# Performance work log

Hardware: AMD Instinct MI355X
Metric: run time of the kernel (lower is better)

The kernel has to match this reference:

```python
import jax, jax.numpy as jnp
import numpy as np

N_NODES = 16384
D_FEAT = 128
HIDDEN = 64
THRESH = 0.85


def setup_inputs() -> dict:
    key = jax.random.key(0)
    kx, kw = jax.random.split(key, 2)
    x = jax.random.normal(kx, (N_NODES, D_FEAT), dtype=jnp.float32)
    # nn.Linear(node_features, hidden_size): weight [H, D], bias [H]
    W = jax.random.normal(kw, (HIDDEN, D_FEAT), dtype=jnp.float32) * 0.05
    b = jnp.zeros((HIDDEN,), dtype=jnp.float32)
    return {"x": x, "W": W, "b": b}


def reference(x, W, b):
    n = x.shape[0]
    # fidelity = (x_i . x_j)^2 for all pairs  -> [n, n]
    fid = jnp.square(x @ x.T)
    # edges exist iff fid >= threshold (weight 1.0); the 0.5-weight elif branch
    # in the original is unreachable. No self-loops (j starts at i+1).
    adj = (fid >= THRESH).astype(x.dtype)
    idx = jnp.arange(n)
    adj = adj.at[idx, idx].set(0.0)
    # weighted neighbor sum per node: [n, d]
    sums = adj @ x
    # original assigns agg[node] = (weights @ neighbor_feats).mean(), a SCALAR
    # broadcast across the feature row; isolated nodes stay zero (their sum
    # row is already zero, so mean is zero -> identical result).
    agg = jnp.broadcast_to(jnp.mean(sums, axis=-1, keepdims=True), x.shape)
    return agg @ W.T + b
```

## Files before the change

kernel.cpp:

```cpp
#include <hip/hip_runtime.h>

#define N_NODES 16384
#define D_FEAT  128
#define HIDDEN  64
#define THRESH  0.85f
#define BAND    0.004f
#define LQCAP   512
#define NBLK    512
#define NT      64

typedef __attribute__((ext_vector_type(8))) short bf16x8;
typedef __attribute__((ext_vector_type(4))) float f32x4;

__device__ __forceinline__ unsigned short f32_to_bf16_rne(float f) {
    unsigned u = __float_as_uint(f);
    unsigned r = (u + 0x7FFFu + ((u >> 16) & 1u)) >> 16;
    return (unsigned short)r;
}

__device__ __forceinline__ void gl_lds16(const unsigned short* src, unsigned short* dst) {
    __builtin_amdgcn_global_load_lds(
        (const __attribute__((address_space(1))) unsigned int*)src,
        (__attribute__((address_space(3))) unsigned int*)dst, 16, 0, 0);
}

__global__ __launch_bounds__(256) void convert_rowsum_kernel(const float* __restrict__ x,
                                                             unsigned short* __restrict__ xhi,
                                                             unsigned short* __restrict__ xlo,
                                                             float* __restrict__ s,
                                                             float* __restrict__ acc,
                                                             int* __restrict__ qcnt) {
    const int tid  = threadIdx.x;
    const int gidx = blockIdx.x * 256 + tid;
    float4 v = ((const float4*)x)[gidx];
    float f[4] = {v.x, v.y, v.z, v.w};
    ushort4 ho, lo;
    unsigned short* hp = &ho.x;
    unsigned short* lp = &lo.x;
    #pragma unroll
    for (int k = 0; k < 4; ++k) {
        unsigned short h = f32_to_bf16_rne(f[k]);
        float hf = __uint_as_float(((unsigned)h) << 16);
        hp[k] = h;
        lp[k] = f32_to_bf16_rne(f[k] - hf);
    }
    ((ushort4*)xhi)[gidx] = ho;
    ((ushort4*)xlo)[gidx] = lo;

    float sum = (v.x + v.y) + (v.z + v.w);
    #pragma unroll
    for (int off = 16; off > 0; off >>= 1) sum += __shfl_xor(sum, off);
    if ((tid & 31) == 0) s[blockIdx.x * 8 + (tid >> 5)] = sum;

    if (tid < 8) acc[blockIdx.x * 8 + tid] = 0.0f;
    if (gidx == 0) *qcnt = 0;
}

__global__ __launch_bounds__(256) void rowsum_kernel(const float* __restrict__ in,
                                                     float* __restrict__ out,
                                                     int nrows) {
    int wave = (blockIdx.x * blockDim.x + threadIdx.x) >> 6;
    int lane = threadIdx.x & 63;
    if (wave >= nrows) return;
    const float2 v = *reinterpret_cast<const float2*>(&in[wave * D_FEAT + lane * 2]);
    float sum = v.x + v.y;
    #pragma unroll
    for (int off = 32; off > 0; off >>= 1) sum += __shfl_down(sum, off, 64);
    if (lane == 0) out[wave] = sum;
}

__global__ __launch_bounds__(256, 2) void pair_mfma(const unsigned short* __restrict__ xhi,
                                                    const unsigned short* __restrict__ xlo,
                                                    const float* __restrict__ s,
                                                    float* __restrict__ acc,
                                                    unsigned* __restrict__ gqueue,
                                                    int* __restrict__ gqcnt) {
    __shared__ unsigned short Bs[3][2][32][128];
    __shared__ float s_lds[2048];
    __shared__ unsigned lq[LQCAP];
    __shared__ int lqcnt, lqbase;

    const int tid  = threadIdx.x;
    const int lane = tid & 63;
    const int w    = tid >> 6;
    const int l15  = lane & 15, l4 = lane >> 4, l7 = lane & 7;

    const int bid = blockIdx.x;
    const int swz = (bid & 7) * 64 + (bid >> 3);
    const int it  = swz & 63;
    const int jc  = swz >> 6;
    const int i0  = it * 256 + w * 64;
    const int jb0 = jc * 2048;

    bf16x8 ahi[4][4], alo[4][4];
    {
        const int abase = (i0 + l15) * D_FEAT + l4 * 8;
        #pragma unroll
        for (int rf = 0; rf < 4; ++rf)
            #pragma unroll
            for (int kc = 0; kc < 4; ++kc) {
                const int off = abase + rf * 16 * D_FEAT + kc * 32;
                ahi[rf][kc] = *(const bf16x8*)(xhi + off);
                alo[rf][kc] = *(const bf16x8*)(xlo + off);
            }
    }

    {
        const float4* sp4 = (const float4*)(s + jb0);
        float4* sl4 = (float4*)s_lds;
        sl4[tid * 2]     = sp4[tid * 2];
        sl4[tid * 2 + 1] = sp4[tid * 2 + 1];
    }
    if (tid == 0) lqcnt = 0;
    __syncthreads();

    int src_off[4]; int dst_off[4]; int plane_sel[4];
    #pragma unroll
    for (int q = 0; q < 4; ++q) {
        const int id = w * 4 + q;
        const int rowt = (id & 7) * 4 + l4;
        plane_sel[q] = id >> 3;
        src_off[q] = rowt * D_FEAT + ((l15 ^ (rowt & 7)) * 8);
        dst_off[q] = (id >> 3) * 4096 + (id & 7) * 512;
    }
    unsigned short* const BsE = &Bs[0][0][0][0];

    #pragma unroll
    for (int tt = 0; tt < 2; ++tt) {
        const int jelem = (jb0 + tt * 32) * D_FEAT;
        #pragma unroll
        for (int q = 0; q < 4; ++q) {
            const unsigned short* sp = (plane_sel[q] ? xlo : xhi) + jelem + src_off[q];
            gl_lds16(sp, BsE + tt * 8192 + dst_off[q]);
        }
    }

    float accf[4][4] = {{0.f}};
    const char* const BsBytes = (const char*)BsE;
    const int rbyte = l15 * 256;
    int swzb[4];
    #pragma unroll
    for (int kc = 0; kc < 4; ++kc) swzb[kc] = (((kc * 4 + l4) ^ l7) * 16);

    int bufc = 0, bufs = 2;
    for (int t = 0; t < NT; ++t) {
        asm volatile("s_waitcnt vmcnt(4)" ::: "memory");
        __builtin_amdgcn_s_barrier();

        {
            const int jelem = (jb0 + ((t + 2) & 63) * 32) * D_FEAT;
            unsigned short* db = BsE + bufs * 8192;
            #pragma unroll
            for (int q = 0; q < 4; ++q) {
                const unsigned short* sp = (plane_sel[q] ? xlo : xhi) + jelem + src_off[q];
                gl_lds16(sp, db + dst_off[q]);
            }
        }

        const int jb = jb0 + t * 32;
        const char* bp = BsBytes + bufc * 16384;

        #pragma unroll
        for (int cg = 0; cg < 2; ++cg) {
            f32x4 C[4];
            #pragma unroll
            for (int rf = 0; rf < 4; ++rf) C[rf] = (f32x4){0.f, 0.f, 0.f, 0.f};

            __builtin_amdgcn_s_setprio(1);
            #pragma unroll
            for (int kc = 0; kc < 4; ++kc) {
                const bf16x8 bh = *(const bf16x8*)(bp + cg * 4096 + rbyte + swzb[kc]);
                const bf16x8 bl = *(const bf16x8*)(bp + 8192 + cg * 4096 + rbyte + swzb[kc]);
                #pragma unroll
                for (int rf = 0; rf < 4; ++rf) {
                    C[rf] = __builtin_amdgcn_mfma_f32_16x16x32_bf16(ahi[rf][kc], bh, C[rf], 0, 0, 0);
                    C[rf] = __builtin_amdgcn_mfma_f32_16x16x32_bf16(alo[rf][kc], bh, C[rf], 0, 0, 0);
                    C[rf] = __builtin_amdgcn_mfma_f32_16x16x32_bf16(ahi[rf][kc], bl, C[rf], 0, 0, 0);
                }
            }
            __builtin_amdgcn_s_setprio(0);

            const int jcol = jb + cg * 16 + l15;
            const float svc = s_lds[t * 32 + cg * 16 + l15];
            #pragma unroll
            for (int rf = 0; rf < 4; ++rf) {
                const int gib = i0 + rf * 16 + l4 * 4;
                #pragma unroll
                for (int r = 0; r < 4; ++r) {
                    const float d = C[rf][r];
                    const float tt = fmaf(d, d, -THRESH);
                    if (fabsf(tt) < BAND) {
                        int p = atomicAdd(&lqcnt, 1);
                        if (p < LQCAP)
                            lq[p] = (((unsigned)(gib + r)) << 14) | (unsigned)jcol;
                    }
                    accf[rf][r] += (tt >= BAND) ? svc : 0.f;
                }
            }
        }

        bufc = (bufc == 2) ? 0 : bufc + 1;
        bufs = (bufs == 2) ? 0 : bufs + 1;
    }

    __syncthreads();

    if (tid == 0) {
        int c = lqcnt; if (c > LQCAP) c = LQCAP;
        lqbase = atomicAdd(gqcnt, c);
        lqcnt = c;
    }
    __syncthreads();
    for (int p = tid; p < lqcnt; p += 256) gqueue[lqbase + p] = lq[p];

    #pragma unroll
    for (int rf = 0; rf < 4; ++rf)
        #pragma unroll
        for (int r = 0; r < 4; ++r) {
            float v = accf[rf][r];
            v += __shfl_xor(v, 1);
            v += __shfl_xor(v, 2);
            v += __shfl_xor(v, 4);
            v += __shfl_xor(v, 8);
            if (l15 == 0) atomicAdd(&acc[i0 + rf * 16 + l4 * 4 + r], v);
        }
}

__global__ __launch_bounds__(256) void fixup_kernel(const unsigned* __restrict__ q,
                                                    const int* __restrict__ qcnt,
                                                    const float* __restrict__ x,
                                                    const float* __restrict__ s,
                                                    float* __restrict__ acc) {
    const int n = *qcnt;
    const int gw = (blockIdx.x * 256 + threadIdx.x) >> 6;
    const int lane = threadIdx.x & 63;
    const int nw = (gridDim.x * 256) >> 6;
    for (int p = gw; p < n; p += nw) {
        const unsigned e = q[p];
        const int i = (int)(e >> 14), j = (int)(e & 16383u);
        const float2 av = ((const float2*)(x + (size_t)i * D_FEAT))[lane];
        const float2 bv = ((const float2*)(x + (size_t)j * D_FEAT))[lane];
        float d = fmaf(av.y, bv.y, av.x * bv.x);
        #pragma unroll
        for (int off = 32; off > 0; off >>= 1) d += __shfl_xor(d, off);
        if (lane == 0) {
            const float tt = fmaf(d, d, -THRESH);
            if (tt >= 0.f) atomicAdd(&acc[i], s[j]);
        }
    }
}

__global__ __launch_bounds__(256) void out_kernel(const float* __restrict__ acc,
                                                  const float* __restrict__ s,
                                                  const float* __restrict__ wsum,
                                                  const float* __restrict__ b,
                                                  float* __restrict__ out) {
    int gid = blockIdx.x * blockDim.x + threadIdx.x;
    int i = gid >> 6;
    int h = gid & 63;
    float a = (acc[i] - s[i]) * (1.0f / 128.0f);
    out[gid] = fmaf(a, wsum[h], b[h]);
}

extern "C" void kernel_launch(void* const* d_in, const int* in_sizes, int n_in,
                              void* d_out, int out_size, void* d_ws, size_t ws_size,
                              hipStream_t stream) {
    const float* x = (const float*)d_in[0];
    const float* W = (const float*)d_in[1];
    const float* b = (const float*)d_in[2];
    float* out = (float*)d_out;

    float*    s     = (float*)d_ws;
    float*    acc   = s + N_NODES;
    float*    wsum  = acc + N_NODES;
    int*      qcnt  = (int*)(wsum + 64);
    unsigned* queue = (unsigned*)(qcnt + 64);
    unsigned short* xhi = (unsigned short*)((char*)d_ws + (2u << 20));
    unsigned short* xlo = (unsigned short*)((char*)d_ws + (6u << 20));

    convert_rowsum_kernel<<<dim3(N_NODES / 8), dim3(256), 0, stream>>>(x, xhi, xlo, s, acc, qcnt);
    rowsum_kernel<<<dim3((HIDDEN * 64 + 255) / 256), dim3(256), 0, stream>>>(W, wsum, HIDDEN);

    pair_mfma<<<dim3(NBLK), dim3(256), 0, stream>>>(xhi, xlo, s, acc, queue, qcnt);
    fixup_kernel<<<dim3(256), dim3(256), 0, stream>>>(queue, qcnt, x, s, acc);
    out_kernel<<<dim3(N_NODES * HIDDEN / 256), dim3(256), 0, stream>>>(acc, s, wsum, b, out);
}
```

Measured before the change: 319.5 us.

## Double-buffer pair tiles, halve column chunk, raise occupancy, fuse W rowsum

Several changes land together. The column chunk per block is halved, so the grid doubles to 1024 blocks, and the LDS ring drops from triple to double buffering with a full vmcnt(0) wait. Launch bounds rise to 4 blocks per CU for more occupancy. The band test now compares |dot| against precomputed bounds instead of d^2-thresh, and a wave-wide __any check skips the queue-push loop when no lane is in the band. The W rowsum kernel is folded into the convert kernel as an extra block, which saves a launch but makes prefetch overlap shallower and may increase register pressure.

```diff
diff --git a/kernel.cpp b/kernel.cpp
--- a/kernel.cpp
+++ b/kernel.cpp
@@ -4,10 +4,13 @@
 #define D_FEAT  128
 #define HIDDEN  64
 #define THRESH  0.85f
-#define BAND    0.004f
+#define DLO     0.91978f
+#define DHI     0.92413f
 #define LQCAP   512
-#define NBLK    512
-#define NT      64
+#define QMAX    450000
+#define NBLK    1024
+#define JCH     1024
+#define NT      32
 
 typedef __attribute__((ext_vector_type(8))) short bf16x8;
 typedef __attribute__((ext_vector_type(4))) float f32x4;
@@ -25,58 +28,59 @@
 }
 
 __global__ __launch_bounds__(256) void convert_rowsum_kernel(const float* __restrict__ x,
+                                                             const float* __restrict__ W,
                                                              unsigned short* __restrict__ xhi,
                                                              unsigned short* __restrict__ xlo,
                                                              float* __restrict__ s,
+                                                             float* __restrict__ wsum,
                                                              float* __restrict__ acc,
                                                              int* __restrict__ qcnt) {
-    const int tid  = threadIdx.x;
-    const int gidx = blockIdx.x * 256 + tid;
-    float4 v = ((const float4*)x)[gidx];
-    float f[4] = {v.x, v.y, v.z, v.w};
-    ushort4 ho, lo;
-    unsigned short* hp = &ho.x;
-    unsigned short* lp = &lo.x;
-    #pragma unroll
-    for (int k = 0; k < 4; ++k) {
-        unsigned short h = f32_to_bf16_rne(f[k]);
-        float hf = __uint_as_float(((unsigned)h) << 16);
-        hp[k] = h;
-        lp[k] = f32_to_bf16_rne(f[k] - hf);
-    }
-    ((ushort4*)xhi)[gidx] = ho;
-    ((ushort4*)xlo)[gidx] = lo;
-
-    float sum = (v.x + v.y) + (v.z + v.w);
-    #pragma unroll
-    for (int off = 16; off > 0; off >>= 1) sum += __shfl_xor(sum, off);
-    if ((tid & 31) == 0) s[blockIdx.x * 8 + (tid >> 5)] = sum;
-
-    if (tid < 8) acc[blockIdx.x * 8 + tid] = 0.0f;
-    if (gidx == 0) *qcnt = 0;
-}
-
-__global__ __launch_bounds__(256) void rowsum_kernel(const float* __restrict__ in,
-                                                     float* __restrict__ out,
-                                                     int nrows) {
-    int wave = (blockIdx.x * blockDim.x + threadIdx.x) >> 6;
-    int lane = threadIdx.x & 63;
-    if (wave >= nrows) return;
-    const float2 v = *reinterpret_cast<const float2*>(&in[wave * D_FEAT + lane * 2]);
-    float sum = v.x + v.y;
-    #pragma unroll
-    for (int off = 32; off > 0; off >>= 1) sum += __shfl_down(sum, off, 64);
-    if (lane == 0) out[wave] = sum;
-}
-
-__global__ __launch_bounds__(256, 2) void pair_mfma(const unsigned short* __restrict__ xhi,
+    const int tid = threadIdx.x;
+    if (blockIdx.x < 2048) {
+        const int gidx = blockIdx.x * 256 + tid;
+        float4 v = ((const float4*)x)[gidx];
+        float f[4] = {v.x, v.y, v.z, v.w};
+        ushort4 ho, lo;
+        unsigned short* hp = &ho.x;
+        unsigned short* lp = &lo.x;
+        #pragma unroll
+        for (int k = 0; k < 4; ++k) {
+            unsigned short h = f32_to_bf16_rne(f[k]);
+            float hf = __uint_as_float(((unsigned)h) << 16);
+            hp[k] = h;
+            lp[k] = f32_to_bf16_rne(f[k] - hf);
+        }
+        ((ushort4*)xhi)[gidx] = ho;
+        ((ushort4*)xlo)[gidx] = lo;
+
+        float sum = (v.x + v.y) + (v.z + v.w);
+        #pragma unroll
+        for (int off = 16; off > 0; off >>= 1) sum += __shfl_xor(sum, off);
+        if ((tid & 31) == 0) s[blockIdx.x * 8 + (tid >> 5)] = sum;
+
+        if (tid < 8) acc[blockIdx.x * 8 + tid] = 0.0f;
+        if (gidx == 0) *qcnt = 0;
+    } else {
+        #pragma unroll
+        for (int p = 0; p < 8; ++p) {
+            const int idx = p * 256 + tid;
+            float4 v = ((const float4*)W)[idx];
+            float sum = (v.x + v.y) + (v.z + v.w);
+            #pragma unroll
+            for (int off = 16; off > 0; off >>= 1) sum += __shfl_xor(sum, off);
+            if ((tid & 31) == 0) wsum[p * 8 + (tid >> 5)] = sum;
+        }
+    }
+}
+
+__global__ __launch_bounds__(256, 4) void pair_mfma(const unsigned short* __restrict__ xhi,
                                                     const unsigned short* __restrict__ xlo,
                                                     const float* __restrict__ s,
                                                     float* __restrict__ acc,
                                                     unsigned* __restrict__ gqueue,
                                                     int* __restrict__ gqcnt) {
-    __shared__ unsigned short Bs[3][2][32][128];
-    __shared__ float s_lds[2048];
+    __shared__ unsigned short Bs[2][2][32][128];
+    __shared__ float s_lds[JCH];
     __shared__ unsigned lq[LQCAP];
     __shared__ int lqcnt, lqbase;
 
@@ -86,11 +90,11 @@
     const int l15  = lane & 15, l4 = lane >> 4, l7 = lane & 7;
 
     const int bid = blockIdx.x;
-    const int swz = (bid & 7) * 64 + (bid >> 3);
+    const int swz = (bid & 7) * 128 + (bid >> 3);
     const int it  = swz & 63;
     const int jc  = swz >> 6;
     const int i0  = it * 256 + w * 64;
-    const int jb0 = jc * 2048;
+    const int jb0 = jc * JCH;
 
     bf16x8 ahi[4][4], alo[4][4];
     {
@@ -105,12 +109,7 @@
             }
     }
 
-    {
-        const float4* sp4 = (const float4*)(s + jb0);
-        float4* sl4 = (float4*)s_lds;
-        sl4[tid * 2]     = sp4[tid * 2];
-        sl4[tid * 2 + 1] = sp4[tid * 2 + 1];
-    }
+    ((float4*)s_lds)[tid] = ((const float4*)(s + jb0))[tid];
     if (tid == 0) lqcnt = 0;
     __syncthreads();
 
@@ -125,13 +124,12 @@
     }
     unsigned short* const BsE = &Bs[0][0][0][0];
 
-    #pragma unroll
-    for (int tt = 0; tt < 2; ++tt) {
-        const int jelem = (jb0 + tt * 32) * D_FEAT;
+    {
+        const int jelem = jb0 * D_FEAT;
         #pragma unroll
         for (int q = 0; q < 4; ++q) {
             const unsigned short* sp = (plane_sel[q] ? xlo : xhi) + jelem + src_off[q];
-            gl_lds16(sp, BsE + tt * 8192 + dst_off[q]);
+            gl_lds16(sp, BsE + dst_off[q]);
         }
     }
 
@@ -142,14 +140,14 @@
     #pragma unroll
     for (int kc = 0; kc < 4; ++kc) swzb[kc] = (((kc * 4 + l4) ^ l7) * 16);
 
-    int bufc = 0, bufs = 2;
+    int buf = 0;
     for (int t = 0; t < NT; ++t) {
-        asm volatile("s_waitcnt vmcnt(4)" ::: "memory");
+        asm volatile("s_waitcnt vmcnt(0)" ::: "memory");
         __builtin_amdgcn_s_barrier();
 
-        {
-            const int jelem = (jb0 + ((t + 2) & 63) * 32) * D_FEAT;
-            unsigned short* db = BsE + bufs * 8192;
+        if (t < NT - 1) {
+            const int jelem = (jb0 + (t + 1) * 32) * D_FEAT;
+            unsigned short* db = BsE + (buf ^ 1) * 8192;
             #pragma unroll
             for (int q = 0; q < 4; ++q) {
                 const unsigned short* sp = (plane_sel[q] ? xlo : xhi) + jelem + src_off[q];
@@ -158,7 +156,7 @@
         }
 
         const int jb = jb0 + t * 32;
-        const char* bp = BsBytes + bufc * 16384;
+        const char* bp = BsBytes + buf * 16384;
 
         #pragma unroll
         for (int cg = 0; cg < 2; ++cg) {
@@ -182,25 +180,30 @@
 
             const int jcol = jb + cg * 16 + l15;
             const float svc = s_lds[t * 32 + cg * 16 + l15];
-            #pragma unroll
-            for (int rf = 0; rf < 4; ++rf) {
-                const int gib = i0 + rf * 16 + l4 * 4;
+            bool anyband = false;
+            #pragma unroll
+            for (int rf = 0; rf < 4; ++rf)
                 #pragma unroll
                 for (int r = 0; r < 4; ++r) {
-                    const float d = C[rf][r];
-                    const float tt = fmaf(d, d, -THRESH);
-                    if (fabsf(tt) < BAND) {
-                        int p = atomicAdd(&lqcnt, 1);
-                        if (p < LQCAP)
-                            lq[p] = (((unsigned)(gib + r)) << 14) | (unsigned)jcol;
+                    const float ad = fabsf(C[rf][r]);
+                    accf[rf][r] += (ad >= DHI) ? svc : 0.f;
+                    anyband = anyband || (ad >= DLO && ad < DHI);
+                }
+            if (__any(anyband)) {
+                #pragma unroll
+                for (int rf = 0; rf < 4; ++rf)
+                    #pragma unroll
+                    for (int r = 0; r < 4; ++r) {
+                        const float ad = fabsf(C[rf][r]);
+                        if (ad >= DLO && ad < DHI) {
+                            int p = atomicAdd(&lqcnt, 1);
+                            if (p < LQCAP)
+                                lq[p] = (((unsigned)(i0 + rf * 16 + l4 * 4 + r)) << 14) | (unsigned)jcol;
+                        }
                     }
-                    accf[rf][r] += (tt >= BAND) ? svc : 0.f;
-                }
-            }
-        }
-
-        bufc = (bufc == 2) ? 0 : bufc + 1;
-        bufs = (bufs == 2) ? 0 : bufs + 1;
+            }
+        }
+        buf ^= 1;
     }
 
     __syncthreads();
@@ -231,7 +234,7 @@
                                                     const float* __restrict__ x,
                                                     const float* __restrict__ s,
                                                     float* __restrict__ acc) {
-    const int n = *qcnt;
+    int n = *qcnt; if (n > QMAX) n = QMAX;
     const int gw = (blockIdx.x * 256 + threadIdx.x) >> 6;
     const int lane = threadIdx.x & 63;
     const int nw = (gridDim.x * 256) >> 6;
@@ -271,16 +274,14 @@
     float* out = (float*)d_out;
 
     float*    s     = (float*)d_ws;
-    float*    acc   = s + N_NODES;
-    float*    wsum  = acc + N_NODES;
-    int*      qcnt  = (int*)(wsum + 64);
-    unsigned* queue = (unsigned*)(qcnt + 64);
+    float*    acc   = (float*)((char*)d_ws + 65536);
+    float*    wsum  = (float*)((char*)d_ws + 131072);
+    int*      qcnt  = (int*)((char*)d_ws + 131328);
+    unsigned* queue = (unsigned*)((char*)d_ws + 262144);
     unsigned short* xhi = (unsigned short*)((char*)d_ws + (2u << 20));
     unsigned short* xlo = (unsigned short*)((char*)d_ws + (6u << 20));
 
-    convert_rowsum_kernel<<<dim3(N_NODES / 8), dim3(256), 0, stream>>>(x, xhi, xlo, s, acc, qcnt);
-    rowsum_kernel<<<dim3((HIDDEN * 64 + 255) / 256), dim3(256), 0, stream>>>(W, wsum, HIDDEN);
-
+    convert_rowsum_kernel<<<dim3(2049), dim3(256), 0, stream>>>(x, W, xhi, xlo, s, wsum, acc, qcnt);
     pair_mfma<<<dim3(NBLK), dim3(256), 0, stream>>>(xhi, xlo, s, acc, queue, qcnt);
     fixup_kernel<<<dim3(256), dim3(256), 0, stream>>>(queue, qcnt, x, s, acc);
     out_kernel<<<dim3(N_NODES * HIDDEN / 256), dim3(256), 0, stream>>>(acc, s, wsum, b, out);
```

New measurement: 895.5 us. 180% more time.
